# Performance work log

Hardware: AMD Instinct MI355X
Metric: run time of the kernel (lower is better)

Reference implementation:

```python
import jax, jax.numpy as jnp
import numpy as np

N_LEVELS = 16
N_FEATS = 2
MIN_RES = 16
MAX_RES = 2048
LOG2_T = 19
T = 1 << LOG2_T  # 524288 hash-table entries per level
B = np.exp((np.log(MAX_RES) - np.log(MIN_RES)) / (N_LEVELS - 1))  # per-level scale ~1.3819
PRIME_Y = np.uint32(2654435761)  # tcnn 2D spatial-hash prime (x prime is 1)
MASK = jnp.uint32(T - 1)


def hash_encode(uv, table):
    """Multiresolution hash-grid encoding (tcnn HashGrid, 2D, bilinear).
    uv: [N,2] in [0,1); table: [L,T,F]. Returns [N, L*F]."""
    outs = []
    for l in range(N_LEVELS):
        scale = MIN_RES * (B ** l) - 1.0          # tcnn grid_scale
        res = int(np.ceil(scale)) + 1             # tcnn grid_resolution
        dense = (res * res) <= T                  # small levels are dense grids
        pos = uv * jnp.float32(scale) + jnp.float32(0.5)
        pg_f = jnp.floor(pos)
        frac = pos - pg_f                          # [N,2] bilinear weights
        pg = pg_f.astype(jnp.uint32)

        def corner_idx(ox, oy):
            x = pg[:, 0] + jnp.uint32(ox)
            y = pg[:, 1] + jnp.uint32(oy)
            if dense:
                return (x + y * jnp.uint32(res)) & MASK
            return (x ^ (y * PRIME_Y)) & MASK

        fx = frac[:, 0:1]
        fy = frac[:, 1:2]
        tl = table[l]
        feat = ((1.0 - fx) * (1.0 - fy) * tl[corner_idx(0, 0)]
                + fx * (1.0 - fy) * tl[corner_idx(1, 0)]
                + (1.0 - fx) * fy * tl[corner_idx(0, 1)]
                + fx * fy * tl[corner_idx(1, 1)])
        outs.append(feat)
    return jnp.concatenate(outs, axis=-1)  # [N, 32]


def mlp(x, w0, w1, w2):
    # FullyFusedMLP: no biases, ReLU hidden, Sigmoid output
    h = jax.nn.relu(x @ w0)
    h = jax.nn.relu(h @ w1)
    return jax.nn.sigmoid(h @ w2)  # [N, 3]


def setup_inputs() -> dict:
    key = jax.random.key(0)
    ks = jax.random.split(key, 5)
    N = 2_097_152
    uv = jax.random.uniform(ks[0], (N, 2), jnp.float32)
    # tcnn HashGrid init: uniform in [-1e-4, 1e-4]
    table = jax.random.uniform(ks[1], (N_LEVELS, T, N_FEATS), jnp.float32, -1e-4, 1e-4)
    w0 = jax.random.normal(ks[2], (32, 64), jnp.float32) * jnp.float32(1.0 / np.sqrt(32))
    w1 = jax.random.normal(ks[3], (64, 64), jnp.float32) * jnp.float32(1.0 / np.sqrt(64))
    w2 = jax.random.normal(ks[4], (64, 3), jnp.float32) * jnp.float32(1.0 / np.sqrt(64))
    return {"uv": uv, "table": table, "w0": w0, "w1": w1, "w2": w2}


def reference(uv, table, w0, w1, w2):
    return mlp(hash_encode(uv, table), w0, w1, w2)
```

## Files before the change

### kernel.cpp

```cpp
#include <hip/hip_runtime.h>
#include <math.h>
#include <stdint.h>

#define NLV 16
#define LOG2T 19
#define TSZ (1u << LOG2T)
#define TMASK (TSZ - 1u)
#define PRIME_Y 2654435761u

#define WP8_BYTES  (4 * 64 * 8)
#define WP16_BYTES (10 * 64 * 16)
#define WPF_BYTES  (WP8_BYTES + WP16_BYTES)

#define FSCALE 8192.0f
#define FUNSCALE (1.0f / 8192.0f)

#define NCOARSE 512
#define P1_PTS 8192
#define P2_CAP 5120

struct NGPParams {
    float scale[NLV];
    unsigned res[NLV];
    unsigned hashed_mask;
};

struct __align__(8) pairld { float x, y, z, w; };

typedef __attribute__((ext_vector_type(8))) short bf16x8;
typedef __attribute__((ext_vector_type(4))) float f32x4;

__device__ inline ushort bf16_rn(float f) {
    uint32_t u = __float_as_uint(f);
    return (ushort)((u + 0x7FFFu + ((u >> 16) & 1u)) >> 16);
}
__device__ inline uint32_t pack_trunc(float a, float b) {
    return __builtin_amdgcn_perm(__float_as_uint(a), __float_as_uint(b), 0x07060302u);
}
__device__ inline ushort cvt_pk_fp8(float a, float b) {
    unsigned r = 0;
    asm("v_cvt_pk_fp8_f32 %0, %1, %2" : "+v"(r) : "v"(a), "v"(b));
    return (ushort)r;
}
__device__ inline unsigned coarse_of(float2 v) {
    unsigned b = (unsigned)(v.y * 512.f); return b > 511u ? 511u : b;
}
__device__ inline unsigned fine_of(float2 v) {
    unsigned b = (unsigned)(v.x * 256.f); return b > 255u ? 255u : b;
}
__device__ inline int xcd_swz(int orig, int nwg) {
    const int q = nwg >> 3, r = nwg & 7;
    const int xcd = orig & 7, k = orig >> 3;
    return (xcd < r ? xcd * (q + 1) : r * (q + 1) + (xcd - r) * q) + k;
}

__global__ __launch_bounds__(256) void ngp_prep_wfrag(
    const float* __restrict__ w0, const float* __restrict__ w1,
    const float* __restrict__ w2,
    unsigned long long* __restrict__ wp8, ushort* __restrict__ wp16)
{
    const int t = threadIdx.x;
    {
        const int f = t >> 6, lane = t & 63;
        const int g4 = lane >> 4, r16 = lane & 15;
        const int nn = f * 16 + r16, k0 = 8 * g4;
        float v[8];
        #pragma unroll
        for (int j = 0; j < 8; ++j) v[j] = w0[(k0 + j) * 64 + nn];
        const unsigned long long p0 = cvt_pk_fp8(v[0], v[1]);
        const unsigned long long p1 = cvt_pk_fp8(v[2], v[3]);
        const unsigned long long p2 = cvt_pk_fp8(v[4], v[5]);
        const unsigned long long p3 = cvt_pk_fp8(v[6], v[7]);
        wp8[f * 64 + lane] = p0 | (p1 << 16) | (p2 << 32) | (p3 << 48);
    }
    for (int i = 0; i < 3; ++i) {
        const int e = t + 256 * i;
        if (e >= 640) continue;
        const int f = e >> 6, lane = e & 63;
        const int g4 = lane >> 4, r16 = lane & 15;
        ushort v[8];
        if (f < 8) {
            const int nn = (f >> 1) * 16 + r16, k0 = (f & 1) * 32 + 8 * g4;
            #pragma unroll
            for (int j = 0; j < 8; ++j) v[j] = bf16_rn(w1[(k0 + j) * 64 + nn]);
        } else {
            const int nn = r16, k0 = (f - 8) * 32 + 8 * g4;
            #pragma unroll
            for (int j = 0; j < 8; ++j)
                v[j] = (nn < 3) ? bf16_rn(w2[(k0 + j) * 3 + nn]) : (ushort)0;
        }
        #pragma unroll
        for (int j = 0; j < 8; ++j) wp16[e * 8 + j] = v[j];
    }
}

__global__ __launch_bounds__(1024) void ngp_hist512(
    const float2* __restrict__ uv, uint32_t* __restrict__ hist, int n)
{
    __shared__ unsigned int h[NCOARSE];
    const int t = threadIdx.x;
    if (t < NCOARSE) h[t] = 0;
    __syncthreads();
    const int b0 = blockIdx.x * P1_PTS;
    #pragma unroll
    for (int k = 0; k < 8; ++k) {
        const int i = b0 + t + k * 1024;
        if (i < n) atomicAdd(&h[coarse_of(uv[i])], 1u);
    }
    __syncthreads();
    if (t < NCOARSE && h[t]) atomicAdd(&hist[t], h[t]);
}

__global__ __launch_bounds__(512) void ngp_scan512(
    const uint32_t* __restrict__ hist, uint32_t* __restrict__ base,
    uint32_t* __restrict__ cursor)
{
    __shared__ unsigned int s[NCOARSE];
    const int t = threadIdx.x;
    const uint32_t mine = hist[t];
    s[t] = mine;
    __syncthreads();
    for (int off = 1; off < NCOARSE; off <<= 1) {
        uint32_t v = (t >= off) ? s[t - off] : 0u;
        __syncthreads();
        s[t] += v;
        __syncthreads();
    }
    const uint32_t excl = s[t] - mine;
    base[t] = excl;
    cursor[t] = excl;
}

__global__ __launch_bounds__(1024) void ngp_pass1(
    const float2* __restrict__ uv, uint32_t* __restrict__ cursor,
    float2* __restrict__ suv, uint32_t* __restrict__ perm, int n)
{
    __shared__ float2       spt[P1_PTS];
    __shared__ unsigned int sid[P1_PTS];
    __shared__ unsigned int hist[NCOARSE], lbase[NCOARSE], lcur[NCOARSE], gbase[NCOARSE];
    __shared__ unsigned int stot;

    const int t = threadIdx.x;
    const int b0 = blockIdx.x * P1_PTS;
    if (t < NCOARSE) hist[t] = 0;
    __syncthreads();

    float2 p[8]; unsigned pc[8];
    #pragma unroll
    for (int k = 0; k < 8; ++k) {
        const int i = b0 + t + k * 1024;
        if (i < n) {
            p[k] = uv[i];
            pc[k] = coarse_of(p[k]);
            atomicAdd(&hist[pc[k]], 1u);
        } else pc[k] = 0xFFFFFFFFu;
    }
    __syncthreads();
    if (t < NCOARSE) lbase[t] = hist[t];
    __syncthreads();
    for (int off = 1; off < NCOARSE; off <<= 1) {
        uint32_t v = 0;
        if (t < NCOARSE && t >= off) v = lbase[t - off];
        __syncthreads();
        if (t < NCOARSE) lbase[t] += v;
        __syncthreads();
    }
    if (t < NCOARSE) {
        const uint32_t excl = lbase[t] - hist[t];
        lcur[t] = excl;
        gbase[t] = atomicAdd(&cursor[t], hist[t]);
        lbase[t] = excl;
        if (t == NCOARSE - 1) stot = excl + hist[t];
    }
    __syncthreads();
    #pragma unroll
    for (int k = 0; k < 8; ++k) {
        if (pc[k] != 0xFFFFFFFFu) {
            const uint32_t r = atomicAdd(&lcur[pc[k]], 1u);
            spt[r] = p[k];
            sid[r] = (unsigned)(b0 + t + k * 1024);
        }
    }
    __syncthreads();
    const uint32_t tot = stot;
    for (uint32_t j = t; j < tot; j += 1024) {
        const float2 v = spt[j];
        const unsigned c = coarse_of(v);
        const uint32_t d = gbase[c] + (j - lbase[c]);
        suv[d] = v;
        perm[d] = sid[j];
    }
}

__global__ __launch_bounds__(1024) void ngp_pass2(
    const uint32_t* __restrict__ basev, const uint32_t* __restrict__ histv,
    float2* __restrict__ suv, uint32_t* __restrict__ perm)
{
    __shared__ float2       spt[P2_CAP];
    __shared__ unsigned int sid[P2_CAP];
    __shared__ unsigned int hist[256], lbase[256], lcur[256];

    const int b = blockIdx.x;
    const uint32_t lo = basev[b];
    const uint32_t cnt = histv[b];
    if (cnt > P2_CAP) return;
    const int t = threadIdx.x;
    if (t < 256) hist[t] = 0;
    __syncthreads();
    for (uint32_t j = t; j < cnt; j += 1024) {
        const float2 v = suv[lo + j];
        spt[j] = v; sid[j] = perm[lo + j];
        atomicAdd(&hist[fine_of(v)], 1u);
    }
    __syncthreads();
    if (t < 256) lbase[t] = hist[t];
    __syncthreads();
    for (int off = 1; off < 256; off <<= 1) {
        uint32_t v = 0;
        if (t < 256 && t >= off) v = lbase[t - off];
        __syncthreads();
        if (t < 256) lbase[t] += v;
        __syncthreads();
    }
    if (t < 256) lcur[t] = lbase[t] - hist[t];
    __syncthreads();
    for (uint32_t j = t; j < cnt; j += 1024) {
        const float2 v = spt[j];
        const uint32_t r = atomicAdd(&lcur[fine_of(v)], 1u);
        suv[lo + r] = v;
        perm[lo + r] = sid[j];
    }
}

__global__ __launch_bounds__(256) void ngp_encode2_kernel(
    const float2* __restrict__ pts,
    const float2* __restrict__ table,
    ushort* __restrict__ xt,
    NGPParams p, int n, int chunks2)
{
    const int bid = blockIdx.x;
    const int pass = bid / chunks2;
    const int chunk = xcd_swz(bid - pass * chunks2, chunks2);
    const int base = chunk * 512 + threadIdx.x;

    float2 xy[2];
    #pragma unroll
    for (int q = 0; q < 2; ++q) {
        int idx = base + q * 256;
        xy[q] = pts[idx < n ? idx : (n - 1)];
    }

    const int l0 = (pass == 0) ? 0 : (pass == 1 ? 10 : 10 + pass);
    const int l1 = (pass == 0) ? 9 : (pass == 1 ? 11 : 10 + pass);

    for (int l = l0; l <= l1; ++l) {
        const float s = p.scale[l];
        const unsigned res = p.res[l];
        const bool hashed = (p.hashed_mask >> l) & 1u;
        const float2* tl = table + ((size_t)l << LOG2T);

        #pragma unroll
        for (int q = 0; q < 2; ++q) {
            const float px = xy[q].x * s + 0.5f;
            const float py = xy[q].y * s + 0.5f;
            const float fpx = floorf(px), fpy = floorf(py);
            const float fx = px - fpx, fy = py - fpy;
            const unsigned x0 = (unsigned)fpx, y0 = (unsigned)fpy;

            float2 c00, c10, c01, c11;
            if (!hashed) {
                const unsigned b0 = x0 + y0 * res;
                const pairld q0 = *(const pairld*)(tl + b0);
                const pairld q1 = *(const pairld*)(tl + b0 + res);
                c00 = make_float2(q0.x, q0.y); c10 = make_float2(q0.z, q0.w);
                c01 = make_float2(q1.x, q1.y); c11 = make_float2(q1.z, q1.w);
            } else {
                const unsigned hy0 = y0 * PRIME_Y;
                const unsigned hy1 = (y0 + 1u) * PRIME_Y;
                if (!(x0 & 1u)) {
                    const unsigned i0 = (x0 ^ hy0) & TMASK;
                    const unsigned i2 = (x0 ^ hy1) & TMASK;
                    const pairld q0 = *(const pairld*)(tl + (i0 & ~1u));
                    const pairld q2 = *(const pairld*)(tl + (i2 & ~1u));
                    if (i0 & 1u) { c00 = make_float2(q0.z, q0.w); c10 = make_float2(q0.x, q0.y); }
                    else         { c00 = make_float2(q0.x, q0.y); c10 = make_float2(q0.z, q0.w); }
                    if (i2 & 1u) { c01 = make_float2(q2.z, q2.w); c11 = make_float2(q2.x, q2.y); }
                    else         { c01 = make_float2(q2.x, q2.y); c11 = make_float2(q2.z, q2.w); }
                } else {
                    c00 = tl[(x0 ^ hy0) & TMASK];
                    c10 = tl[((x0 + 1u) ^ hy0) & TMASK];
                    c01 = tl[(x0 ^ hy1) & TMASK];
                    c11 = tl[((x0 + 1u) ^ hy1) & TMASK];
                }
            }

            const float w00 = (1.f - fx) * (1.f - fy);
            const float w10 = fx * (1.f - fy);
            const float w01 = (1.f - fx) * fy;
            const float w11 = fx * fy;
            const float f0 = w00 * c00.x + w10 * c10.x + w01 * c01.x + w11 * c11.x;
            const float f1 = w00 * c00.y + w10 * c10.y + w01 * c01.y + w11 * c11.y;
            const ushort pk = cvt_pk_fp8(f0 * FSCALE, f1 * FSCALE);
            const int idx = base + q * 256;
            if (idx < n) xt[(size_t)l * n + idx] = pk;
        }
    }
}

__global__ __launch_bounds__(256, 4) void ngp_mlp_persist(
    const ushort* __restrict__ xt,
    const unsigned long long* __restrict__ wp8,
    const ushort* __restrict__ wp16,
    const uint32_t* __restrict__ perm,
    float* __restrict__ out, int n, int nchunks)
{
    __shared__ __align__(16) ushort H[256 * 72];

    const int t = threadIdx.x;
    const int lane = t & 63;
    const int w = t >> 6;
    const int g4 = lane >> 4;
    const int r16 = lane & 15;

    unsigned long long wf8[4];
    #pragma unroll
    for (int f = 0; f < 4; ++f) wf8[f] = wp8[f * 64 + lane];
    bf16x8 wf16[10];
    #pragma unroll
    for (int f = 0; f < 10; ++f)
        wf16[f] = *(const bf16x8*)(wp16 + (size_t)(f * 64 + lane) * 8);

    for (int c = blockIdx.x; c < nchunks; c += gridDim.x) {
        const int pbase = c << 8;
        #pragma unroll
        for (int mi = 0; mi < 4; ++mi) {
            const int plocal = (w * 4 + mi) * 16 + r16;
            int pg = pbase + plocal;
            pg = pg < n ? pg : n - 1;
            union { ushort s[4]; unsigned long long v; } xv;
            #pragma unroll
            for (int c4 = 0; c4 < 4; ++c4)
                xv.s[c4] = xt[(size_t)(4 * g4 + c4) * n + pg];
            f32x4 a[4];
            #pragma unroll
            for (int nt = 0; nt < 4; ++nt)
                a[nt] = __builtin_amdgcn_mfma_f32_16x16x32_fp8_fp8(
                    (long)wf8[nt], (long)xv.v, (f32x4){0.f, 0.f, 0.f, 0.f}, 0, 0, 0);
            const int pl = plocal * 72;
            #pragma unroll
            for (int nt = 0; nt < 4; ++nt) {
                const uint32_t d0 = pack_trunc(fmaxf(a[nt][1] * FUNSCALE, 0.f),
                                               fmaxf(a[nt][0] * FUNSCALE, 0.f));
                const uint32_t d1 = pack_trunc(fmaxf(a[nt][3] * FUNSCALE, 0.f),
                                               fmaxf(a[nt][2] * FUNSCALE, 0.f));
                *(uint2*)&H[pl + nt * 16 + 4 * g4] = make_uint2(d0, d1);
            }
        }
        #pragma unroll
        for (int mi = 0; mi < 4; ++mi) {
            const int plocal = (w * 4 + mi) * 16 + r16;
            const int pl = plocal * 72;
            const bf16x8 bh0 = *(const bf16x8*)&H[pl + 8 * g4];
            const bf16x8 bh1 = *(const bf16x8*)&H[pl + 32 + 8 * g4];
            #pragma unroll
            for (int nt = 0; nt < 4; ++nt) {
                f32x4 acc = __builtin_amdgcn_mfma_f32_16x16x32_bf16(
                    wf16[nt * 2], bh0, (f32x4){0.f, 0.f, 0.f, 0.f}, 0, 0, 0);
                acc = __builtin_amdgcn_mfma_f32_16x16x32_bf16(
                    wf16[nt * 2 + 1], bh1, acc, 0, 0, 0);
                const uint32_t d0 = pack_trunc(fmaxf(acc[1], 0.f), fmaxf(acc[0], 0.f));
                const uint32_t d1 = pack_trunc(fmaxf(acc[3], 0.f), fmaxf(acc[2], 0.f));
                *(uint2*)&H[pl + nt * 16 + 4 * g4] = make_uint2(d0, d1);
            }
            const bf16x8 ch0 = *(const bf16x8*)&H[pl + 8 * g4];
            const bf16x8 ch1 = *(const bf16x8*)&H[pl + 32 + 8 * g4];
            f32x4 z = __builtin_amdgcn_mfma_f32_16x16x32_bf16(
                wf16[8], ch0, (f32x4){0.f, 0.f, 0.f, 0.f}, 0, 0, 0);
            z = __builtin_amdgcn_mfma_f32_16x16x32_bf16(wf16[9], ch1, z, 0, 0, 0);
            if (g4 == 0) {
                const int pgs = pbase + plocal;
                if (pgs < n) {
                    const int pg = perm ? (int)perm[pgs] : pgs;
                    #pragma unroll
                    for (int r = 0; r < 3; ++r)
                        out[(size_t)pg * 3 + r] = 1.f / (1.f + __expf(-z[r]));
                }
            }
        }
    }
}

__global__ __launch_bounds__(256) void ngp_fused_kernel(
    const float2* __restrict__ uv,
    const float2* __restrict__ table,
    const float4* __restrict__ w0,
    const float4* __restrict__ w1,
    const float*  __restrict__ w2,
    float* __restrict__ out,
    NGPParams p, int n)
{
    __shared__ float4 sw0[512];
    __shared__ float4 sw1[1024];
    __shared__ float  sw2[192];
    const int t = threadIdx.x;
    #pragma unroll
    for (int i = 0; i < 2; i++) sw0[t + 256 * i] = w0[t + 256 * i];
    #pragma unroll
    for (int i = 0; i < 4; i++) sw1[t + 256 * i] = w1[t + 256 * i];
    if (t < 192) sw2[t] = w2[t];
    __syncthreads();
    const int gi = blockIdx.x * 256 + t;
    if (gi >= n) return;
    const float2 xy = uv[gi];
    float feat[32];
    #pragma unroll
    for (int l = 0; l < NLV; l++) {
        const float s = p.scale[l];
        const unsigned res = p.res[l];
        const float px = xy.x * s + 0.5f;
        const float py = xy.y * s + 0.5f;
        const float fpx = floorf(px), fpy = floorf(py);
        const float fx = px - fpx, fy = py - fpy;
        const unsigned x0 = (unsigned)fpx, y0 = (unsigned)fpy;
        unsigned i00, i10, i01, i11;
        if (!((p.hashed_mask >> l) & 1u)) {
            const unsigned b = x0 + y0 * res;
            i00 = b & TMASK; i10 = (b + 1u) & TMASK;
            i01 = (b + res) & TMASK; i11 = (b + res + 1u) & TMASK;
        } else {
            const unsigned hy0 = y0 * PRIME_Y;
            const unsigned hy1 = (y0 + 1u) * PRIME_Y;
            i00 = (x0 ^ hy0) & TMASK; i10 = ((x0 + 1u) ^ hy0) & TMASK;
            i01 = (x0 ^ hy1) & TMASK; i11 = ((x0 + 1u) ^ hy1) & TMASK;
        }
        const float2* tl = table + ((size_t)l << LOG2T);
        const float2 c00 = tl[i00], c10 = tl[i10], c01 = tl[i01], c11 = tl[i11];
        const float w00 = (1.f - fx) * (1.f - fy);
        const float w10 = fx * (1.f - fy);
        const float w01 = (1.f - fx) * fy;
        const float w11 = fx * fy;
        feat[2 * l]     = w00 * c00.x + w10 * c10.x + w01 * c01.x + w11 * c11.x;
        feat[2 * l + 1] = w00 * c00.y + w10 * c10.y + w01 * c01.y + w11 * c11.y;
    }
    float2 h0[32];
    #pragma unroll
    for (int j = 0; j < 32; j++) h0[j] = make_float2(0.f, 0.f);
    #pragma unroll
    for (int k = 0; k < 32; k++) {
        const float f = feat[k];
        #pragma unroll
        for (int j = 0; j < 16; j++) {
            const float4 ww = sw0[k * 16 + j];
            h0[2 * j].x = fmaf(f, ww.x, h0[2 * j].x);
            h0[2 * j].y = fmaf(f, ww.y, h0[2 * j].y);
            h0[2 * j + 1].x = fmaf(f, ww.z, h0[2 * j + 1].x);
            h0[2 * j + 1].y = fmaf(f, ww.w, h0[2 * j + 1].y);
        }
    }
    #pragma unroll
    for (int j = 0; j < 32; j++) {
        h0[j].x = fmaxf(h0[j].x, 0.f);
        h0[j].y = fmaxf(h0[j].y, 0.f);
    }
    float2 h1[32];
    #pragma unroll
    for (int j = 0; j < 32; j++) h1[j] = make_float2(0.f, 0.f);
    #pragma unroll
    for (int k = 0; k < 64; k++) {
        const float f = (k & 1) ? h0[k >> 1].y : h0[k >> 1].x;
        #pragma unroll
        for (int j = 0; j < 16; j++) {
            const float4 ww = sw1[k * 16 + j];
            h1[2 * j].x = fmaf(f, ww.x, h1[2 * j].x);
            h1[2 * j].y = fmaf(f, ww.y, h1[2 * j].y);
            h1[2 * j + 1].x = fmaf(f, ww.z, h1[2 * j + 1].x);
            h1[2 * j + 1].y = fmaf(f, ww.w, h1[2 * j + 1].y);
        }
    }
    #pragma unroll
    for (int j = 0; j < 32; j++) {
        h1[j].x = fmaxf(h1[j].x, 0.f);
        h1[j].y = fmaxf(h1[j].y, 0.f);
    }
    float z0 = 0.f, z1 = 0.f, z2 = 0.f;
    #pragma unroll
    for (int k = 0; k < 64; k++) {
        const float f = (k & 1) ? h1[k >> 1].y : h1[k >> 1].x;
        z0 = fmaf(f, sw2[3 * k + 0], z0);
        z1 = fmaf(f, sw2[3 * k + 1], z1);
        z2 = fmaf(f, sw2[3 * k + 2], z2);
    }
    out[3 * gi + 0] = 1.f / (1.f + __expf(-z0));
    out[3 * gi + 1] = 1.f / (1.f + __expf(-z1));
    out[3 * gi + 2] = 1.f / (1.f + __expf(-z2));
}

extern "C" void kernel_launch(void* const* d_in, const int* in_sizes, int n_in,
                              void* d_out, int out_size, void* d_ws, size_t ws_size,
                              hipStream_t stream) {
    const float2* uv    = (const float2*)d_in[0];
    const float2* table = (const float2*)d_in[1];
    const float*  w0f   = (const float*)d_in[2];
    const float*  w1f   = (const float*)d_in[3];
    const float*  w2f   = (const float*)d_in[4];
    float* out = (float*)d_out;

    const int n = in_sizes[0] / 2;

    NGPParams p;
    p.hashed_mask = 0;
    const double B = exp((log(2048.0) - log(16.0)) / 15.0);
    for (int l = 0; l < NLV; l++) {
        const double scale = 16.0 * pow(B, (double)l) - 1.0;
        const long long res = (long long)ceil(scale) + 1;
        p.scale[l] = (float)scale;
        p.res[l] = (unsigned)res;
        if (res * res > (long long)TSZ) p.hashed_mask |= (1u << l);
    }

    const size_t xt_bytes   = (size_t)NLV * (size_t)n * 2u;
    const size_t wpf_bytes  = ((size_t)WPF_BYTES + 63u) & ~63ull;
    const size_t suv_bytes  = (size_t)n * 8u;
    const size_t perm_bytes = (size_t)n * 4u;
    const size_t ctl_bytes  = (size_t)NCOARSE * 4u * 3u;

    const size_t need_sorted = xt_bytes + wpf_bytes + suv_bytes + perm_bytes + ctl_bytes;
    const size_t need_plain  = xt_bytes + wpf_bytes;

    const int chunks  = (n + 255) / 256;
    const int chunks2 = (n + 511) / 512;

    if (ws_size < need_plain) {
        ngp_fused_kernel<<<chunks, 256, 0, stream>>>(
            uv, table, (const float4*)w0f, (const float4*)w1f, w2f, out, p, n);
        return;
    }

    ushort* xt = (ushort*)d_ws;
    unsigned long long* wp8 = (unsigned long long*)((char*)d_ws + xt_bytes);
    ushort* wp16 = (ushort*)((char*)d_ws + xt_bytes + WP8_BYTES);
    ngp_prep_wfrag<<<1, 256, 0, stream>>>(w0f, w1f, w2f, wp8, wp16);

    const int mlp_blocks = chunks < 1024 ? chunks : 1024;

    if (ws_size < need_sorted) {
        ngp_encode2_kernel<<<6 * chunks2, 256, 0, stream>>>(uv, table, xt, p, n, chunks2);
        ngp_mlp_persist<<<mlp_blocks, 256, 0, stream>>>(xt, wp8, wp16,
                                                        (const uint32_t*)nullptr, out, n, chunks);
        return;
    }

    float2*   suv    = (float2*)((char*)d_ws + xt_bytes + wpf_bytes);
    uint32_t* perm   = (uint32_t*)((char*)suv + suv_bytes);
    uint32_t* hist   = (uint32_t*)((char*)perm + perm_bytes);
    uint32_t* basev  = hist + NCOARSE;
    uint32_t* cursor = basev + NCOARSE;

    const int p1_blocks = (n + P1_PTS - 1) / P1_PTS;

    hipMemsetAsync(hist, 0, (size_t)NCOARSE * 4u, stream);
    ngp_hist512<<<p1_blocks, 1024, 0, stream>>>(uv, hist, n);
    ngp_scan512<<<1, NCOARSE, 0, stream>>>(hist, basev, cursor);
    ngp_pass1<<<p1_blocks, 1024, 0, stream>>>(uv, cursor, suv, perm, n);
    ngp_pass2<<<NCOARSE, 1024, 0, stream>>>(basev, hist, suv, perm);
    ngp_encode2_kernel<<<6 * chunks2, 256, 0, stream>>>(suv, table, xt, p, n, chunks2);
    ngp_mlp_persist<<<mlp_blocks, 256, 0, stream>>>(xt, wp8, wp16, perm, out, n, chunks);
}
```

Baseline: 175.6 us.

## Fuse sort passes into one cooperative kernel and map MLP chunks per XCD

Replaces the four-kernel counting sort (histogram, scan, scatter, fine bucket sort) with a single cooperative kernel. It keeps each block's points in shared memory and uses grid-wide syncs in place of kernel boundaries, so uv is read once instead of twice and the small-kernel launch gaps go away. It also reassigns MLP chunks so that blocks on the same XCD handle a contiguous range, which is meant to improve L2 locality. The cost is two grid syncs, a fixed 256-block residency requirement, and large per-block shared memory of about 80KB at 1024 threads, which may limit co-residency.

```diff
diff --git a/kernel.cpp b/kernel.cpp
--- a/kernel.cpp
+++ b/kernel.cpp
@@ -1,6 +1,9 @@
 #include <hip/hip_runtime.h>
+#include <hip/hip_cooperative_groups.h>
 #include <math.h>
 #include <stdint.h>
+
+namespace cg = cooperative_groups;
 
 #define NLV 16
 #define LOG2T 19
@@ -91,6 +94,114 @@
         }
         #pragma unroll
         for (int j = 0; j < 8; ++j) wp16[e * 8 + j] = v[j];
+    }
+}
+
+__global__ __launch_bounds__(1024) void ngp_sort_coop(
+    const float2* __restrict__ uv, uint32_t* __restrict__ cursor,
+    float2* __restrict__ suv, uint32_t* __restrict__ perm, int n)
+{
+    __shared__ float2       spt[P1_PTS];
+    __shared__ unsigned int sid[P1_PTS];
+    __shared__ unsigned int h[NCOARSE], lbase[NCOARSE], lcur[NCOARSE];
+    __shared__ unsigned int gbase[NCOARSE], excl[NCOARSE];
+    __shared__ unsigned int stot;
+
+    const int t = threadIdx.x;
+    const int b0 = blockIdx.x * P1_PTS;
+    cg::grid_group grid = cg::this_grid();
+
+    if (t < NCOARSE) h[t] = 0;
+    __syncthreads();
+    float2 p[8]; unsigned pc[8];
+    #pragma unroll
+    for (int k = 0; k < 8; ++k) {
+        const int i = b0 + t + k * 1024;
+        if (i < n) {
+            p[k] = uv[i];
+            pc[k] = coarse_of(p[k]);
+            atomicAdd(&h[pc[k]], 1u);
+        } else pc[k] = 0xFFFFFFFFu;
+    }
+    __syncthreads();
+    if (t < NCOARSE) gbase[t] = h[t] ? atomicAdd(&cursor[t], h[t]) : 0u;
+
+    grid.sync();
+
+    uint32_t tot = 0;
+    if (t < NCOARSE) { tot = cursor[t]; excl[t] = tot; }
+    __syncthreads();
+    for (int off = 1; off < NCOARSE; off <<= 1) {
+        uint32_t v = 0;
+        if (t < NCOARSE && t >= off) v = excl[t - off];
+        __syncthreads();
+        if (t < NCOARSE) excl[t] += v;
+        __syncthreads();
+    }
+    if (t < NCOARSE) excl[t] -= tot;
+    if (t < NCOARSE) lbase[t] = h[t];
+    __syncthreads();
+    for (int off = 1; off < NCOARSE; off <<= 1) {
+        uint32_t v = 0;
+        if (t < NCOARSE && t >= off) v = lbase[t - off];
+        __syncthreads();
+        if (t < NCOARSE) lbase[t] += v;
+        __syncthreads();
+    }
+    if (t == NCOARSE - 1) stot = lbase[t];
+    if (t < NCOARSE) { lbase[t] -= h[t]; lcur[t] = lbase[t]; }
+    __syncthreads();
+    #pragma unroll
+    for (int k = 0; k < 8; ++k) {
+        if (pc[k] != 0xFFFFFFFFu) {
+            const uint32_t r = atomicAdd(&lcur[pc[k]], 1u);
+            spt[r] = p[k];
+            sid[r] = (unsigned)(b0 + t + k * 1024);
+        }
+    }
+    __syncthreads();
+    const uint32_t tt = stot;
+    for (uint32_t j = t; j < tt; j += 1024) {
+        const float2 v = spt[j];
+        const unsigned c = coarse_of(v);
+        const uint32_t d = excl[c] + gbase[c] + (j - lbase[c]);
+        suv[d] = v;
+        perm[d] = sid[j];
+    }
+
+    grid.sync();
+
+    for (int sidx = blockIdx.x; sidx < NCOARSE; sidx += gridDim.x) {
+        __syncthreads();
+        const uint32_t lo = excl[sidx];
+        const uint32_t hi = (sidx + 1 < NCOARSE) ? excl[sidx + 1] : (uint32_t)n;
+        const uint32_t cnt = hi - lo;
+        if (cnt > (uint32_t)P1_PTS) continue;
+        if (t < 256) h[t] = 0;
+        __syncthreads();
+        for (uint32_t j = t; j < cnt; j += 1024) {
+            const float2 v = suv[lo + j];
+            spt[j] = v; sid[j] = perm[lo + j];
+            atomicAdd(&h[fine_of(v)], 1u);
+        }
+        __syncthreads();
+        if (t < 256) lbase[t] = h[t];
+        __syncthreads();
+        for (int off = 1; off < 256; off <<= 1) {
+            uint32_t v = 0;
+            if (t < 256 && t >= off) v = lbase[t - off];
+            __syncthreads();
+            if (t < 256) lbase[t] += v;
+            __syncthreads();
+        }
+        if (t < 256) lcur[t] = lbase[t] - h[t];
+        __syncthreads();
+        for (uint32_t j = t; j < cnt; j += 1024) {
+            const float2 v = spt[j];
+            const uint32_t r = atomicAdd(&lcur[fine_of(v)], 1u);
+            suv[lo + r] = v;
+            perm[lo + r] = sid[j];
+        }
     }
 }
 
@@ -330,7 +441,7 @@
     for (int f = 0; f < 10; ++f)
         wf16[f] = *(const bf16x8*)(wp16 + (size_t)(f * 64 + lane) * 8);
 
-    for (int c = blockIdx.x; c < nchunks; c += gridDim.x) {
+    auto body = [&](int c) {
         const int pbase = c << 8;
         #pragma unroll
         for (int mi = 0; mi < 4; ++mi) {
@@ -387,6 +498,16 @@
                 }
             }
         }
+    };
+
+    if ((gridDim.x & 7) == 0 && (nchunks & 7) == 0) {
+        const int cpx = nchunks >> 3;
+        const int bpb = gridDim.x >> 3;
+        const int xcd = blockIdx.x & 7;
+        const int local = blockIdx.x >> 3;
+        for (int k = local; k < cpx; k += bpb) body(xcd * cpx + k);
+    } else {
+        for (int c = blockIdx.x; c < nchunks; c += gridDim.x) body(c);
     }
 }
 
@@ -552,17 +673,26 @@
 
     float2*   suv    = (float2*)((char*)d_ws + xt_bytes + wpf_bytes);
     uint32_t* perm   = (uint32_t*)((char*)suv + suv_bytes);
-    uint32_t* hist   = (uint32_t*)((char*)perm + perm_bytes);
+    uint32_t* cursor = (uint32_t*)((char*)perm + perm_bytes);
+    uint32_t* hist   = cursor + NCOARSE;
     uint32_t* basev  = hist + NCOARSE;
-    uint32_t* cursor = basev + NCOARSE;
 
     const int p1_blocks = (n + P1_PTS - 1) / P1_PTS;
 
-    hipMemsetAsync(hist, 0, (size_t)NCOARSE * 4u, stream);
-    ngp_hist512<<<p1_blocks, 1024, 0, stream>>>(uv, hist, n);
-    ngp_scan512<<<1, NCOARSE, 0, stream>>>(hist, basev, cursor);
-    ngp_pass1<<<p1_blocks, 1024, 0, stream>>>(uv, cursor, suv, perm, n);
-    ngp_pass2<<<NCOARSE, 1024, 0, stream>>>(basev, hist, suv, perm);
+    if (p1_blocks <= 256) {
+        hipMemsetAsync(cursor, 0, (size_t)NCOARSE * 4u, stream);
+        float2* uv_nc = (float2*)uv;
+        void* args[] = { (void*)&uv_nc, (void*)&cursor, (void*)&suv,
+                         (void*)&perm, (void*)&n };
+        hipLaunchCooperativeKernel((void*)ngp_sort_coop, dim3(p1_blocks),
+                                   dim3(1024), args, 0, stream);
+    } else {
+        hipMemsetAsync(hist, 0, (size_t)NCOARSE * 4u, stream);
+        ngp_hist512<<<p1_blocks, 1024, 0, stream>>>(uv, hist, n);
+        ngp_scan512<<<1, NCOARSE, 0, stream>>>(hist, basev, cursor);
+        ngp_pass1<<<p1_blocks, 1024, 0, stream>>>(uv, cursor, suv, perm, n);
+        ngp_pass2<<<NCOARSE, 1024, 0, stream>>>(basev, hist, suv, perm);
+    }
     ngp_encode2_kernel<<<6 * chunks2, 256, 0, stream>>>(suv, table, xt, p, n, chunks2);
     ngp_mlp_persist<<<mlp_blocks, 256, 0, stream>>>(xt, wp8, wp16, perm, out, n, chunks);
 }
```

Result: slower. 240.8 us (+37.1%).
